# Kernel tuning notes

Hardware: AMD Instinct MI355X
Metric: run time of the kernel (lower is better)

Reference implementation:

```python
import jax, jax.numpy as jnp
import numpy as np
from jax import lax

EPS = 1e-20
BN_EPS = 1e-5
ATTN_SCALE = 2.8284271247461903  # sqrt(d_l=8)
NS = (32, 32, 32, 10)
DS = (8, 8, 8, 16)


def squash(x):
    # Efficient-CapsNet squash: (1 - 1/(exp(||x||)+eps)) * x/(||x||+eps)
    norm = jnp.linalg.norm(x, axis=-1, keepdims=True)
    return (1.0 - 1.0 / (jnp.exp(norm) + EPS)) * (x / (norm + EPS))


def conv2d(x, w, b, stride, groups=1):
    y = lax.conv_general_dilated(
        x, w, window_strides=(stride, stride), padding='VALID',
        dimension_numbers=('NCHW', 'OIHW', 'NCHW'),
        feature_group_count=groups)
    return y + b[None, :, None, None]


def bn(x, g, b, m, v):
    inv = g / jnp.sqrt(v + BN_EPS)
    return x * inv[None, :, None, None] + (b - m * inv)[None, :, None, None]


def fccaps(U_l, W):
    # U_l: (b, n_l, d_l), W: (n_l, n_h, d_l, d_h)
    U_hat = jnp.einsum('bij,ikjl->bikl', U_l, W)          # (b, n_l, n_h, d_h)
    A = jnp.einsum('bikl,bhkl->bhik', U_hat, U_hat)        # (b, n_l, n_l, n_h)
    A_sum = jnp.sum(A, axis=-2)                            # (b, n_l, n_h)
    C = jax.nn.softmax(A_sum / ATTN_SCALE, axis=-1)        # (b, n_l, n_h)
    U_h = jnp.einsum('bikl,bik->bkl', U_hat, C)            # (b, n_h, d_h)
    return squash(U_h)


def setup_inputs() -> dict:
    key = jax.random.key(0)
    ks = jax.random.split(key, 8)
    B = 512
    x = jax.random.normal(ks[0], (B, 1, 39, 39), dtype=jnp.float32)
    conv1_w = jax.random.normal(ks[1], (128, 1, 3, 3), jnp.float32) * 0.2
    conv1_b = jnp.zeros((128,), jnp.float32)
    conv2_w = jax.random.normal(ks[2], (256, 128, 3, 3), jnp.float32) * 0.04
    conv2_b = jnp.zeros((256,), jnp.float32)
    conv3_w = jax.random.normal(ks[3], (256, 1, 9, 9), jnp.float32) * 0.1  # depthwise
    conv3_b = jnp.zeros((256,), jnp.float32)
    bn1_g = jnp.ones((128,), jnp.float32); bn1_b = jnp.zeros((128,), jnp.float32)
    bn1_m = jnp.zeros((128,), jnp.float32); bn1_v = jnp.ones((128,), jnp.float32)
    bn2_g = jnp.ones((256,), jnp.float32); bn2_b = jnp.zeros((256,), jnp.float32)
    bn2_m = jnp.zeros((256,), jnp.float32); bn2_v = jnp.ones((256,), jnp.float32)
    # capsule weights, kaiming-ish scale sqrt(2/fan_in) with fan_in = n_h*d_l*d_h
    def caps_w(k, n_l, n_h, d_l, d_h):
        std = np.sqrt(2.0 / (n_h * d_l * d_h))
        return jax.random.normal(k, (n_l, n_h, d_l, d_h), jnp.float32) * std
    W1 = caps_w(ks[4], NS[0], NS[1], DS[0], DS[1])
    W2 = caps_w(ks[5], NS[1], NS[2], DS[1], DS[2])
    W3 = caps_w(ks[6], NS[2], NS[3], DS[2], DS[3])
    return dict(x=x, conv1_w=conv1_w, conv1_b=conv1_b,
                bn1_g=bn1_g, bn1_b=bn1_b, bn1_m=bn1_m, bn1_v=bn1_v,
                conv2_w=conv2_w, conv2_b=conv2_b,
                bn2_g=bn2_g, bn2_b=bn2_b, bn2_m=bn2_m, bn2_v=bn2_v,
                conv3_w=conv3_w, conv3_b=conv3_b, W1=W1, W2=W2, W3=W3)


def reference(x, conv1_w, conv1_b, bn1_g, bn1_b, bn1_m, bn1_v,
              conv2_w, conv2_b, bn2_g, bn2_b, bn2_m, bn2_v,
              conv3_w, conv3_b, W1, W2, W3):
    h = jax.nn.relu(bn(conv2d(x, conv1_w, conv1_b, 2), bn1_g, bn1_b, bn1_m, bn1_v))
    h = jax.nn.relu(bn(conv2d(h, conv2_w, conv2_b, 2), bn2_g, bn2_b, bn2_m, bn2_v))
    h = conv2d(h, conv3_w, conv3_b, 1, groups=256)        # (B, 256, 1, 1)
    u = h.reshape(h.shape[0], NS[0], DS[0])                # (B, 32, 8)
    u = squash(u)
    for W in (W1, W2, W3):
        u = fccaps(u, W)
    return u  # (B, 10, 16)
```

## Files before the change

### kernel.cpp

```cpp
#include <hip/hip_runtime.h>


typedef __attribute__((ext_vector_type(8))) short short8;
typedef __attribute__((ext_vector_type(4))) float f32x4;

__device__ __forceinline__ ushort f2bf(float x) {
    uint u = __float_as_uint(x);
    return (ushort)((u + 0x7FFFu + ((u >> 16) & 1u)) >> 16);
}
__device__ __forceinline__ void bfsplit(float x, ushort& h, ushort& l) {
    h = f2bf(x);
    float hf = __uint_as_float(((uint)h) << 16);
    l = f2bf(x - hf);
}

__global__ __launch_bounds__(256) void k_prep(
    const float* __restrict__ w2, uint* __restrict__ Bt,
    const float* __restrict__ w3, float* __restrict__ w3T,
    const float* __restrict__ W1, const float* __restrict__ W2,
    const float* __restrict__ W3, float* __restrict__ Wr1,
    float* __restrict__ Wr2, float* __restrict__ Wr3,
    const float* __restrict__ c1b, const float* __restrict__ g1,
    const float* __restrict__ b1, const float* __restrict__ m1,
    const float* __restrict__ v1, float2* __restrict__ sc1) {
    __shared__ __align__(16) float wbuf[64 * 288];
    const int b = blockIdx.x, t = threadIdx.x;
    if (b < 144) {
        const int sidx = b >> 2, coq = b & 3;
        const int chunk = sidx / 9, tap = sidx - chunk * 9;
        const int co0 = coq * 64;
        for (int idx = t; idx < 4608; idx += 256) {
            const int n = idx / 72, q = idx - n * 72;
            ((float4*)wbuf)[n * 72 + q] =
                *(const float4*)(w2 + (size_t)(co0 + n) * 1152 + chunk * 288 + q * 4);
        }
        __syncthreads();
        const int n = t & 63, dg = (t >> 6) * 4;
        const int cot = coq >> 1, nn = ((coq & 1) * 64) + n;
        uint* dst = Bt + (size_t)(sidx * 2 + cot) * 4096;
#pragma unroll
        for (int dd = 0; dd < 4; ++dd) {
            const int d = dg + dd;
            const float x = wbuf[n * 288 + (2 * d) * 9 + tap];
            const float y = wbuf[n * 288 + (2 * d + 1) * 9 + tap];
            ushort xh, xl, yh, yl;
            bfsplit(x, xh, xl);
            bfsplit(y, yh, yl);
            dst[nn * 16 + d]        = (uint)xh | ((uint)yh << 16);
            dst[2048 + nn * 16 + d] = (uint)xl | ((uint)yl << 16);
        }
    } else if (b < 225) {
        const int p = b - 144;
        w3T[p * 256 + t] = w3[t * 81 + p];
    } else if (b < 321) {
        const int bb = b - 225;
        const int layer = bb >> 5, blk = bb & 31;
        const float* src = layer == 0 ? W1 : (layer == 1 ? W2 : W3);
        float* dst = layer == 0 ? Wr1 : (layer == 1 ? Wr2 : Wr3);
        const int d_h = (layer == 2) ? 16 : 8;
        const int total = (layer == 2) ? 5120 : 8192;
        for (int idx = blk * 256 + t; idx < 8 * total; idx += 32 * 256) {
            const int e = idx >> 3, j = idx & 7;
            const int ik = e / d_h, l = e - ik * d_h;
            dst[idx] = src[(ik * 8 + j) * d_h + l];
        }
    } else {
        if (t < 128) {
            const float inv = g1[t] * rsqrtf(v1[t] + 1e-5f);
            sc1[t] = make_float2(inv, c1b[t] * inv + b1[t] - m1[t] * inv);
        }
    }
}

__device__ __forceinline__ void fccaps512(
    const int n_l, const int n_h, const int d_h, const float* __restrict__ Wr,
    const float* Vin, const float* cIn, float* Uh, float* Sv, float* Av,
    float* Cv, float* coefs, float* outG, const int t) {
    const int nkd = n_h * d_h;
    const int total = n_l * nkd;
    __syncthreads();
    for (int e = t; e < total; e += 512) {
        const int i = e / nkd;
        const float4* w4 = (const float4*)(Wr + (size_t)e * 8);
        const float4 wa = w4[0], wb = w4[1];
        const float4* u4 = (const float4*)(Vin + i * 8);
        const float4 ua = u4[0], ub = u4[1];
        Uh[e] = cIn[i] *
                (ua.x * wa.x + ua.y * wa.y + ua.z * wa.z + ua.w * wa.w +
                 ub.x * wb.x + ub.y * wb.y + ub.z * wb.z + ub.w * wb.w);
    }
    __syncthreads();
    for (int e = t; e < nkd; e += 512) {
        float acc = 0.0f;
        for (int i = 0; i < n_l; ++i) acc += Uh[i * nkd + e];
        Sv[e] = acc;
    }
    __syncthreads();
    for (int e = t; e < n_l * n_h; e += 512) {
        const int h = e / n_h, k = e - h * n_h;
        float acc = 0.0f;
        for (int l = 0; l < d_h; ++l)
            acc += Uh[h * nkd + k * d_h + l] * Sv[k * d_h + l];
        Av[e] = acc;
    }
    __syncthreads();
    {
        const int h = t >> 3, sub = t & 7;
        if (h < n_l) {
            const float invs = 1.0f / 2.8284271247461903f;
            float mx = -1e30f;
            for (int k = sub; k < n_h; k += 8) mx = fmaxf(mx, Av[h * n_h + k]);
            mx = fmaxf(mx, __shfl_xor(mx, 1));
            mx = fmaxf(mx, __shfl_xor(mx, 2));
            mx = fmaxf(mx, __shfl_xor(mx, 4));
            float sum = 0.0f;
            for (int k = sub; k < n_h; k += 8) {
                const float ev = expf((Av[h * n_h + k] - mx) * invs);
                Cv[h * n_h + k] = ev;
                sum += ev;
            }
            sum += __shfl_xor(sum, 1);
            sum += __shfl_xor(sum, 2);
            sum += __shfl_xor(sum, 4);
            const float r = 1.0f / sum;
            for (int k = sub; k < n_h; k += 8) Cv[h * n_h + k] *= r;
        }
    }
    __syncthreads();
    for (int e = t; e < nkd; e += 512) {
        const int k = e / d_h;
        float acc = 0.0f;
        for (int i = 0; i < n_l; ++i) acc += Uh[i * nkd + e] * Cv[i * n_h + k];
        Sv[e] = acc;
    }
    __syncthreads();
    if (t < n_h) {
        float ssq = 0.0f;
        for (int l = 0; l < d_h; ++l) { const float uv = Sv[t * d_h + l]; ssq += uv * uv; }
        const float n = sqrtf(ssq);
        coefs[t] = (1.0f - 1.0f / (expf(n) + 1e-20f)) / (n + 1e-20f);
    }
    if (outG) {
        __syncthreads();
        for (int e = t; e < nkd; e += 512) outG[e] = Sv[e] * coefs[e / d_h];
    }
}

__global__ __launch_bounds__(512, 4) void k_conv2(
    const float* __restrict__ x, const float* __restrict__ w1,
    const float2* __restrict__ sc1, const uint* __restrict__ Bt,
    const float* __restrict__ g,
    const float* __restrict__ bb, const float* __restrict__ bm,
    const float* __restrict__ bv, const float* __restrict__ bias,
    const float* __restrict__ w3T, const float* __restrict__ b3,
    const float* __restrict__ Wr1, const float* __restrict__ Wr2,
    const float* __restrict__ Wr3, float* __restrict__ out) {
    __shared__ __align__(16) uint raw[11552];
    __shared__ __align__(16) float xs[1560];
    __shared__ float ured[256];
    const int t = threadIdx.x;
    const int lane = t & 63, wave = t >> 6;
    const int ln15 = lane & 15, lq = lane >> 4;
    const int wm = (wave >> 2) * 48;
    const int wn = (wave & 3) * 64;
    const int cot_w = (wave & 3) >> 1;
    const int bi = blockIdx.x;

    const float* xb = x + (size_t)bi * 1521;
    for (int i = t; i < 1521; i += 512) {
        const int y = i / 39, xc = i - y * 39;
        xs[y * 40 + xc] = xb[i];
    }

    const int qc = t & 15, ol = qc >> 2, qo = (qc & 3) * 2, pg = t >> 4;

    int PE[3], PO[3];
#pragma unroll
    for (int i = 0; i < 3; ++i) {
        const int m = wm + i * 16 + ln15;
        const int p = m < 81 ? m : 80;
        const int oh = p / 9, ow = p - oh * 9;
        PE[i] = lq * 760 + oh * 80 + ow * 4;
        PO[i] = 3040 + lq * 684 + oh * 72 + ow * 4;
    }
    int BRDg[4];
#pragma unroll
    for (int j = 0; j < 4; ++j) {
        const int n = ((wn & 64) + j * 16 + ln15);
        BRDg[j] = n * 16 + lq * 4;
    }

    f32x4 acc[3][4] = {};

#pragma unroll
    for (int c = 0; c < 4; ++c) {
        const int o_g = c * 32 + qc * 2;
        float wr[18];
        {
            const float2* wp = reinterpret_cast<const float2*>(w1 + o_g * 9);
#pragma unroll
            for (int q = 0; q < 9; ++q) {
                const float2 wv = wp[q];
                wr[q * 2] = wv.x; wr[q * 2 + 1] = wv.y;
            }
        }
        float2 ssv[2];
        ssv[0] = sc1[o_g];
        ssv[1] = sc1[o_g + 1];

        __syncthreads();

        {
            ushort* rawu = (ushort*)raw;
            for (int p = pg; p < 361; p += 32) {
                const int y = p / 19, xq = p - y * 19;
                const int b2 = y * 80 + xq * 2;
                const float2 x01 = *(const float2*)(xs + b2);
                const float  x2v = xs[b2 + 2];
                const float2 x34 = *(const float2*)(xs + b2 + 40);
                const float  x5v = xs[b2 + 42];
                const float2 x67 = *(const float2*)(xs + b2 + 80);
                const float  x8v = xs[b2 + 82];
                uint hw, lw;
                {
                    uint hv[2], lv[2];
#pragma unroll
                    for (int jj = 0; jj < 2; ++jj) {
                        const float a = x01.x * wr[jj * 9 + 0] + x01.y * wr[jj * 9 + 1] +
                                        x2v   * wr[jj * 9 + 2] + x34.x * wr[jj * 9 + 3] +
                                        x34.y * wr[jj * 9 + 4] + x5v   * wr[jj * 9 + 5] +
                                        x67.x * wr[jj * 9 + 6] + x67.y * wr[jj * 9 + 7] +
                                        x8v   * wr[jj * 9 + 8];
                        const float v = fmaxf(fmaf(a, ssv[jj].x, ssv[jj].y), 0.0f);
                        const uint u = __float_as_uint(v);
                        hv[jj] = u >> 16;
                        const float d = v - __uint_as_float(u & 0xFFFF0000u);
                        lv[jj] = __float_as_uint(d) >> 16;
                    }
                    hw = hv[0] | (hv[1] << 16);
                    lw = lv[0] | (lv[1] << 16);
                }
                int ad;
                if ((xq & 1) == 0) {
                    ad = ol * 1520 + (y * 10 + (xq >> 1)) * 8 + qo;
                } else {
                    ad = 6080 + ol * 1368 + (y * 9 + (xq >> 1)) * 8 + qo;
                }
                *(uint*)(rawu + ad)         = hw;
                *(uint*)(rawu + 11552 + ad) = lw;
            }
        }
        __syncthreads();

#pragma unroll
        for (int tap = 0; tap < 9; ++tap) {
            const int s = c * 9 + tap;
            const int kh = tap / 3, kw = tap - kh * 3;
            const int odd = kw & 1;
            const int sE = kh * 40 + (kw >> 1) * 4;
            const int sO = kh * 36;
            short8 a_h[3], a_l[3];
#pragma unroll
            for (int i = 0; i < 3; ++i) {
                const int addr = odd ? (PO[i] + sO) : (PE[i] + sE);
                a_h[i] = *reinterpret_cast<const short8*>(raw + addr);
                a_l[i] = *reinterpret_cast<const short8*>(raw + addr + 5776);
            }
            const uint* bp = Bt + (size_t)(s * 2 + cot_w) * 4096;
#pragma unroll
            for (int jh = 0; jh < 2; ++jh) {
                uint4 Bc[4];
#pragma unroll
                for (int j2 = 0; j2 < 2; ++j2) {
                    Bc[j2]     = *(const uint4*)(bp + BRDg[jh * 2 + j2]);
                    Bc[2 + j2] = *(const uint4*)(bp + 2048 + BRDg[jh * 2 + j2]);
                }
                short8 bh[2], bl[2];
#pragma unroll
                for (int j2 = 0; j2 < 2; ++j2) {
                    bh[j2] = __builtin_bit_cast(short8, Bc[j2]);
                    bl[j2] = __builtin_bit_cast(short8, Bc[2 + j2]);
                }
#pragma unroll
                for (int i = 0; i < 3; ++i)
#pragma unroll
                    for (int j2 = 0; j2 < 2; ++j2)
                        acc[i][jh * 2 + j2] = __builtin_amdgcn_mfma_f32_16x16x32_bf16(
                            a_h[i], bh[j2], acc[i][jh * 2 + j2], 0, 0, 0);
#pragma unroll
                for (int i = 0; i < 3; ++i)
#pragma unroll
                    for (int j2 = 0; j2 < 2; ++j2)
                        acc[i][jh * 2 + j2] = __builtin_amdgcn_mfma_f32_16x16x32_bf16(
                            a_h[i], bl[j2], acc[i][jh * 2 + j2], 0, 0, 0);
#pragma unroll
                for (int i = 0; i < 3; ++i)
#pragma unroll
                    for (int j2 = 0; j2 < 2; ++j2)
                        acc[i][jh * 2 + j2] = __builtin_amdgcn_mfma_f32_16x16x32_bf16(
                            a_l[i], bh[j2], acc[i][jh * 2 + j2], 0, 0, 0);
            }
        }
    }

    float scj[4], shj[4];
#pragma unroll
    for (int j = 0; j < 4; ++j) {
        const int co = wn + j * 16 + ln15;
        const float inv = g[co] * rsqrtf(bv[co] + 1e-5f);
        scj[j] = inv;
        shj[j] = bias[co] * inv + bb[co] - bm[co] * inv;
    }
    float usum[4] = {0.f, 0.f, 0.f, 0.f};
#pragma unroll
    for (int i = 0; i < 3; ++i)
#pragma unroll
        for (int r = 0; r < 4; ++r) {
            const int m = wm + i * 16 + lq * 4 + r;
            if (m < 81) {
                const float* wrow = w3T + m * 256;
#pragma unroll
                for (int j = 0; j < 4; ++j) {
                    const int col = wn + j * 16 + ln15;
                    const float v = fmaxf(fmaf(acc[i][j][r], scj[j], shj[j]), 0.0f);
                    usum[j] = fmaf(v, wrow[col], usum[j]);
                }
            }
        }
#pragma unroll
    for (int j = 0; j < 4; ++j) {
        usum[j] += __shfl_xor(usum[j], 16);
        usum[j] += __shfl_xor(usum[j], 32);
    }
    if (lq == 0 && wm == 0) {
#pragma unroll
        for (int j = 0; j < 4; ++j) ured[wn + j * 16 + ln15] = usum[j];
    }
    __syncthreads();

    float* cF    = (float*)raw;
    float* Uh    = cF + 256;
    float* Sv    = cF + 8448;
    float* Av    = cF + 8704;
    float* Cv    = cF + 9728;
    float* coefs = cF + 10752;

    if (lq == 0 && wm == 48) {
#pragma unroll
        for (int j = 0; j < 4; ++j) {
            const int col = wn + j * 16 + ln15;
            cF[col] = usum[j] + ured[col] + b3[col];
        }
    }
    __syncthreads();
    if (t < 32) {
        float ssq = 0.0f;
        for (int j = 0; j < 8; ++j) { const float uv = cF[t * 8 + j]; ssq += uv * uv; }
        const float n = sqrtf(ssq);
        coefs[t] = (1.0f - 1.0f / (expf(n) + 1e-20f)) / (n + 1e-20f);
    }

    fccaps512(32, 32,  8, Wr1, cF, coefs, Uh, Sv, Av, Cv, coefs, nullptr, t);
    fccaps512(32, 32,  8, Wr2, Sv, coefs, Uh, Sv, Av, Cv, coefs, nullptr, t);
    fccaps512(32, 10, 16, Wr3, Sv, coefs, Uh, Sv, Av, Cv, coefs,
              out + (size_t)bi * 160, t);
}

extern "C" void kernel_launch(void* const* d_in, const int* in_sizes, int n_in,
                              void* d_out, int out_size, void* d_ws, size_t ws_size,
                              hipStream_t stream) {
    const float* x    = (const float*)d_in[0];
    const float* c1w  = (const float*)d_in[1];
    const float* c1b  = (const float*)d_in[2];
    const float* bn1g = (const float*)d_in[3];
    const float* bn1b = (const float*)d_in[4];
    const float* bn1m = (const float*)d_in[5];
    const float* bn1v = (const float*)d_in[6];
    const float* c2w  = (const float*)d_in[7];
    const float* c2b  = (const float*)d_in[8];
    const float* bn2g = (const float*)d_in[9];
    const float* bn2b = (const float*)d_in[10];
    const float* bn2m = (const float*)d_in[11];
    const float* bn2v = (const float*)d_in[12];
    const float* c3w  = (const float*)d_in[13];
    const float* c3b  = (const float*)d_in[14];
    const float* W1   = (const float*)d_in[15];
    const float* W2   = (const float*)d_in[16];
    const float* W3   = (const float*)d_in[17];
    float* out = (float*)d_out;
    uint*  wsu = (uint*)d_ws;
    float* wsf = (float*)d_ws;

    uint*   Bt  = wsu + 131072;
    float*  w3T = wsf + 425984;
    float*  Wr1 = wsf + 446720;
    float*  Wr2 = wsf + 512256;
    float*  Wr3 = wsf + 577792;
    float2* sc1 = (float2*)(wsf + 618752);

    k_prep<<<dim3(322), 256, 0, stream>>>(c2w, Bt, c3w, w3T, W1, W2, W3,
                                          Wr1, Wr2, Wr3,
                                          c1b, bn1g, bn1b, bn1m, bn1v, sc1);
    k_conv2<<<dim3(512), 512, 0, stream>>>(x, c1w, sc1, Bt,
                                           bn2g, bn2b, bn2m, bn2v,
                                           c2b, w3T, c3b, Wr1, Wr2, Wr3, out);
}
```

Baseline: 196.7 us.

## Run capsule routing on a single wavefront and drop block barriers

```diff
diff --git a/kernel.cpp b/kernel.cpp
--- a/kernel.cpp
+++ b/kernel.cpp
@@ -3,6 +3,8 @@
 
 typedef __attribute__((ext_vector_type(8))) short short8;
 typedef __attribute__((ext_vector_type(4))) float f32x4;
+
+#define WFENCE() asm volatile("s_waitcnt lgkmcnt(0)" ::: "memory")
 
 __device__ __forceinline__ ushort f2bf(float x) {
     uint u = __float_as_uint(x);
@@ -72,14 +74,14 @@
     }
 }
 
-__device__ __forceinline__ void fccaps512(
+__device__ __forceinline__ void fccaps_wave(
     const int n_l, const int n_h, const int d_h, const float* __restrict__ Wr,
     const float* Vin, const float* cIn, float* Uh, float* Sv, float* Av,
-    float* Cv, float* coefs, float* outG, const int t) {
+    float* Cv, float* coefs, float* outG, const int lane) {
     const int nkd = n_h * d_h;
     const int total = n_l * nkd;
-    __syncthreads();
-    for (int e = t; e < total; e += 512) {
+    for (int e0 = 0; e0 < total; e0 += 64) {
+        const int e = e0 + lane;
         const int i = e / nkd;
         const float4* w4 = (const float4*)(Wr + (size_t)e * 8);
         const float4 wa = w4[0], wb = w4[1];
@@ -89,60 +91,72 @@
                 (ua.x * wa.x + ua.y * wa.y + ua.z * wa.z + ua.w * wa.w +
                  ub.x * wb.x + ub.y * wb.y + ub.z * wb.z + ub.w * wb.w);
     }
-    __syncthreads();
-    for (int e = t; e < nkd; e += 512) {
+    WFENCE();
+    for (int e0 = 0; e0 < nkd; e0 += 64) {
+        const int e = e0 + lane;
+        if (e < nkd) {
+            float acc = 0.0f;
+            for (int i = 0; i < n_l; ++i) acc += Uh[i * nkd + e];
+            Sv[e] = acc;
+        }
+    }
+    WFENCE();
+    for (int e0 = 0; e0 < n_l * n_h; e0 += 64) {
+        const int e = e0 + lane;
+        const int h = e / n_h, k = e - h * n_h;
+        const float4* uh4 = (const float4*)(Uh + h * nkd + k * d_h);
+        const float4* sv4 = (const float4*)(Sv + k * d_h);
         float acc = 0.0f;
-        for (int i = 0; i < n_l; ++i) acc += Uh[i * nkd + e];
-        Sv[e] = acc;
-    }
-    __syncthreads();
-    for (int e = t; e < n_l * n_h; e += 512) {
-        const int h = e / n_h, k = e - h * n_h;
-        float acc = 0.0f;
-        for (int l = 0; l < d_h; ++l)
-            acc += Uh[h * nkd + k * d_h + l] * Sv[k * d_h + l];
+#pragma unroll
+        for (int q = 0; q < 4; ++q) {
+            if (q < d_h / 4) {
+                const float4 a = uh4[q], b = sv4[q];
+                acc += a.x * b.x + a.y * b.y + a.z * b.z + a.w * b.w;
+            }
+        }
         Av[e] = acc;
     }
-    __syncthreads();
+    WFENCE();
     {
-        const int h = t >> 3, sub = t & 7;
-        if (h < n_l) {
-            const float invs = 1.0f / 2.8284271247461903f;
-            float mx = -1e30f;
-            for (int k = sub; k < n_h; k += 8) mx = fmaxf(mx, Av[h * n_h + k]);
-            mx = fmaxf(mx, __shfl_xor(mx, 1));
-            mx = fmaxf(mx, __shfl_xor(mx, 2));
-            mx = fmaxf(mx, __shfl_xor(mx, 4));
-            float sum = 0.0f;
-            for (int k = sub; k < n_h; k += 8) {
-                const float ev = expf((Av[h * n_h + k] - mx) * invs);
-                Cv[h * n_h + k] = ev;
-                sum += ev;
-            }
-            sum += __shfl_xor(sum, 1);
-            sum += __shfl_xor(sum, 2);
-            sum += __shfl_xor(sum, 4);
-            const float r = 1.0f / sum;
-            for (int k = sub; k < n_h; k += 8) Cv[h * n_h + k] *= r;
-        }
-    }
-    __syncthreads();
-    for (int e = t; e < nkd; e += 512) {
-        const int k = e / d_h;
-        float acc = 0.0f;
-        for (int i = 0; i < n_l; ++i) acc += Uh[i * nkd + e] * Cv[i * n_h + k];
-        Sv[e] = acc;
-    }
-    __syncthreads();
-    if (t < n_h) {
+        const int h = lane >> 1, sub = lane & 1;
+        const float invs = 1.0f / 2.8284271247461903f;
+        float mx = -1e30f;
+        for (int k = sub; k < n_h; k += 2) mx = fmaxf(mx, Av[h * n_h + k]);
+        mx = fmaxf(mx, __shfl_xor(mx, 1));
+        float sum = 0.0f;
+        for (int k = sub; k < n_h; k += 2) {
+            const float ev = expf((Av[h * n_h + k] - mx) * invs);
+            Cv[h * n_h + k] = ev;
+            sum += ev;
+        }
+        sum += __shfl_xor(sum, 1);
+        const float r = 1.0f / sum;
+        for (int k = sub; k < n_h; k += 2) Cv[h * n_h + k] *= r;
+    }
+    WFENCE();
+    for (int e0 = 0; e0 < nkd; e0 += 64) {
+        const int e = e0 + lane;
+        if (e < nkd) {
+            const int k = e / d_h;
+            float acc = 0.0f;
+            for (int i = 0; i < n_l; ++i)
+                acc += Uh[i * nkd + e] * Cv[i * n_h + k];
+            Sv[e] = acc;
+        }
+    }
+    WFENCE();
+    if (lane < n_h) {
         float ssq = 0.0f;
-        for (int l = 0; l < d_h; ++l) { const float uv = Sv[t * d_h + l]; ssq += uv * uv; }
+        for (int l = 0; l < d_h; ++l) { const float uv = Sv[lane * d_h + l]; ssq += uv * uv; }
         const float n = sqrtf(ssq);
-        coefs[t] = (1.0f - 1.0f / (expf(n) + 1e-20f)) / (n + 1e-20f);
-    }
+        coefs[lane] = (1.0f - 1.0f / (expf(n) + 1e-20f)) / (n + 1e-20f);
+    }
+    WFENCE();
     if (outG) {
-        __syncthreads();
-        for (int e = t; e < nkd; e += 512) outG[e] = Sv[e] * coefs[e / d_h];
+        for (int e0 = 0; e0 < nkd; e0 += 64) {
+            const int e = e0 + lane;
+            if (e < nkd) outG[e] = Sv[e] * coefs[e / d_h];
+        }
     }
 }
 
@@ -353,17 +367,21 @@
         }
     }
     __syncthreads();
-    if (t < 32) {
+
+    if (wave != 0) return;
+
+    if (lane < 32) {
         float ssq = 0.0f;
-        for (int j = 0; j < 8; ++j) { const float uv = cF[t * 8 + j]; ssq += uv * uv; }
+        for (int j = 0; j < 8; ++j) { const float uv = cF[lane * 8 + j]; ssq += uv * uv; }
         const float n = sqrtf(ssq);
-        coefs[t] = (1.0f - 1.0f / (expf(n) + 1e-20f)) / (n + 1e-20f);
-    }
-
-    fccaps512(32, 32,  8, Wr1, cF, coefs, Uh, Sv, Av, Cv, coefs, nullptr, t);
-    fccaps512(32, 32,  8, Wr2, Sv, coefs, Uh, Sv, Av, Cv, coefs, nullptr, t);
-    fccaps512(32, 10, 16, Wr3, Sv, coefs, Uh, Sv, Av, Cv, coefs,
-              out + (size_t)bi * 160, t);
+        coefs[lane] = (1.0f - 1.0f / (expf(n) + 1e-20f)) / (n + 1e-20f);
+    }
+    WFENCE();
+
+    fccaps_wave(32, 32,  8, Wr1, cF, coefs, Uh, Sv, Av, Cv, coefs, nullptr, lane);
+    fccaps_wave(32, 32,  8, Wr2, Sv, coefs, Uh, Sv, Av, Cv, coefs, nullptr, lane);
+    fccaps_wave(32, 10, 16, Wr3, Sv, coefs, Uh, Sv, Av, Cv, coefs,
+                out + (size_t)bi * 160, lane);
 }
 
 extern "C" void kernel_launch(void* const* d_in, const int* in_sizes, int n_in,
```

Result: slower. 228.2 us (+16.0%).
